# Kernel optimization log

Hardware: AMD Instinct MI355X
Metric: run time of the kernel (lower is better)

## Reference

```python
import jax, jax.numpy as jnp
import numpy as np
import math

D_MODEL = 1024
NUM_HEADS = 16
D_K = D_MODEL // NUM_HEADS
THETA = 10000.0
BATCH = 2
SEQ = 2048


def _trunc_normal(key, shape, std):
    # truncated normal in [-3std, 3std], matching torch.nn.init.trunc_normal_
    return jax.random.truncated_normal(key, -3.0, 3.0, shape, jnp.float32) * std


def setup_inputs() -> dict:
    key = jax.random.key(0)
    kx, kq, kk, kv, ko = jax.random.split(key, 5)
    std = math.sqrt(2.0 / (D_MODEL + D_MODEL))
    return {
        "x": jax.random.normal(kx, (BATCH, SEQ, D_MODEL), jnp.float32),
        "Wq": _trunc_normal(kq, (D_MODEL, D_MODEL), std),
        "Wk": _trunc_normal(kk, (D_MODEL, D_MODEL), std),
        "Wv": _trunc_normal(kv, (D_MODEL, D_MODEL), std),
        "Wo": _trunc_normal(ko, (D_MODEL, D_MODEL), std),
    }


def _apply_rope(t):
    # t: [B, H, S, d_k]; positions = arange(S)
    S = t.shape[-2]
    inv_freq = 1.0 / THETA ** (jnp.arange(0, D_K, 2, dtype=jnp.float32) / D_K)
    ang = jnp.arange(S, dtype=jnp.float32)[:, None] * inv_freq[None, :]  # [S, d_k/2]
    cos, sin = jnp.cos(ang), jnp.sin(ang)
    t1 = t[..., ::2]
    t2 = t[..., 1::2]
    r1 = t1 * cos - t2 * sin
    r2 = t1 * sin + t2 * cos
    # interleave back: even indices <- r1, odd <- r2
    out = jnp.stack([r1, r2], axis=-1).reshape(t.shape)
    return out


def reference(x, Wq, Wk, Wv, Wo):
    B, S, _ = x.shape
    def proj(W):
        return (x @ W.T).reshape(B, S, NUM_HEADS, D_K).transpose(0, 2, 1, 3)
    q = _apply_rope(proj(Wq))
    k = _apply_rope(proj(Wk))
    v = proj(Wv)
    scores = jnp.einsum('bhqd,bhkd->bhqk', q, k) / math.sqrt(D_K)
    causal = jnp.tril(jnp.ones((S, S), dtype=bool))
    scores = jnp.where(causal, scores, -jnp.inf)
    attn = jax.nn.softmax(scores, axis=-1)
    ctx = jnp.einsum('bhqk,bhkd->bhqd', attn, v)  # [B,H,S,d_k]
    ctx = ctx.transpose(0, 2, 1, 3).reshape(B, S, D_MODEL)
    return ctx @ Wo.T
```

## Files before the change

kernel.cpp:

```cpp
#include <hip/hip_runtime.h>
#include <hip/hip_bf16.h>


typedef __attribute__((ext_vector_type(8))) short bf16x8;
typedef __attribute__((ext_vector_type(4))) short bf16x4;
typedef __attribute__((ext_vector_type(4))) float f32x4;

#define D_MODEL 1024
#define SEQ     2048
#define NHEAD   16
#define DK      64
#define EXP_BIAS 16.0f

__device__ __forceinline__ f32x4 mfma16(bf16x8 a, bf16x8 b, f32x4 c) {
    return __builtin_amdgcn_mfma_f32_16x16x32_bf16(a, b, c, 0, 0, 0);
}

__device__ __forceinline__ void load_lds16(const __hip_bfloat16* g, __hip_bfloat16* l) {
    __builtin_amdgcn_global_load_lds((const __attribute__((address_space(1))) void*)g,
                                     (__attribute__((address_space(3))) void*)l,
                                     16, 0, 0);
}

__device__ __forceinline__ void cvt8(const float* p, __hip_bfloat16* dst) {
    const float4 f0 = *(const float4*)p;
    const float4 f1 = *(const float4*)(p + 4);
    alignas(16) __hip_bfloat16 t[8] = {
        __float2bfloat16(f0.x), __float2bfloat16(f0.y),
        __float2bfloat16(f0.z), __float2bfloat16(f0.w),
        __float2bfloat16(f1.x), __float2bfloat16(f1.y),
        __float2bfloat16(f1.z), __float2bfloat16(f1.w)};
    *(bf16x8*)dst = *(const bf16x8*)t;
}

__global__ __launch_bounds__(256) void cvt5_k(const float* __restrict__ wq,
                                              const float* __restrict__ wk,
                                              const float* __restrict__ wv,
                                              const float* __restrict__ wo,
                                              const float* __restrict__ x,
                                              __hip_bfloat16* __restrict__ dw,
                                              __hip_bfloat16* __restrict__ dwo,
                                              __hip_bfloat16* __restrict__ dx) {
    const int id = blockIdx.x;
    const float* s;
    __hip_bfloat16* d;
    int off;
    if (id < 1536)      { const int w = id >> 9; s = (w == 0) ? wq : (w == 1 ? wk : wv);
                          d = dw + (size_t)w * 1024 * 1024; off = (id & 511) * 2048; }
    else if (id < 2048) { s = wo; d = dwo; off = (id - 1536) * 2048; }
    else                { s = x;  d = dx;  off = (id - 2048) * 2048; }
    const int i = off + threadIdx.x * 8;
    alignas(16) __hip_bfloat16 t[8];
    cvt8(s + i, t);
    *(bf16x8*)(d + i) = *(const bf16x8*)t;
}

__global__ __launch_bounds__(256) void cvt3_k(const float* __restrict__ s0,
                                              const float* __restrict__ s1,
                                              const float* __restrict__ s2,
                                              __hip_bfloat16* __restrict__ d0,
                                              __hip_bfloat16* __restrict__ d1,
                                              __hip_bfloat16* __restrict__ d2) {
    const float* s = (blockIdx.y == 0) ? s0 : (blockIdx.y == 1 ? s1 : s2);
    __hip_bfloat16* d = (blockIdx.y == 0) ? d0 : (blockIdx.y == 1 ? d1 : d2);
    const int i = (blockIdx.x * 256 + threadIdx.x) * 8;
    alignas(16) __hip_bfloat16 t[8];
    cvt8(s + i, t);
    *(bf16x8*)(d + i) = *(const bf16x8*)t;
}

__device__ __forceinline__ void qkv_epilogue(f32x4 (&acc)[4][4], int wsel,
                                             int bm, int bn, int wave,
                                             int quad, int l15,
                                             __hip_bfloat16* Cq,
                                             __hip_bfloat16* Ck,
                                             __hip_bfloat16* Vt) {
    if (wsel < 2) {
        __hip_bfloat16* C = (wsel == 0) ? Cq : Ck;
#pragma unroll
        for (int i = 0; i < 4; ++i)
#pragma unroll
            for (int j = 0; j < 4; ++j)
#pragma unroll
                for (int r = 0; r < 4; ++r) {
                    const int row = bm + (wave >> 1) * 64 + i * 16 + quad * 4 + r;
                    const int col = bn + (wave & 1) * 64 + j * 16 + l15;
                    C[(size_t)row * 1024 + col] = __float2bfloat16(acc[i][j][r]);
                }
    } else {
#pragma unroll
        for (int i = 0; i < 4; ++i)
#pragma unroll
            for (int j = 0; j < 4; ++j) {
                const int col  = bn + (wave & 1) * 64 + j * 16 + l15;
                const int hh   = col >> 6, dd = col & 63;
                const int row0 = bm + (wave >> 1) * 64 + i * 16 + quad * 4;
                const int bb   = row0 >> 11, s0 = row0 & 2047;
                alignas(8) __hip_bfloat16 t4[4] = {
                    __float2bfloat16(acc[i][j][0]), __float2bfloat16(acc[i][j][1]),
                    __float2bfloat16(acc[i][j][2]), __float2bfloat16(acc[i][j][3])};
                *(uint2*)&Vt[((size_t)(bb * 16 + hh) * 64 + dd) * 2048 + s0] =
                    *(const uint2*)t4;
            }
    }
}

__global__ __launch_bounds__(256) void gemm_qkv_bf(const __hip_bfloat16* __restrict__ X,
                                                   const __hip_bfloat16* __restrict__ W,
                                                   __hip_bfloat16* __restrict__ Cq,
                                                   __hip_bfloat16* __restrict__ Ck,
                                                   __hip_bfloat16* __restrict__ Vt) {
    __shared__ alignas(16) __hip_bfloat16 a_lds[128 * 32];
    __shared__ alignas(16) __hip_bfloat16 b_lds[128 * 32];

    const int tid  = threadIdx.x;
    const int wave = tid >> 6;
    const int lane = tid & 63;
    const int quad = lane >> 4;
    const int l15  = lane & 15;

    const int wsel = blockIdx.x >> 3;
    const int bn   = (blockIdx.x & 7) * 128;
    const int bm   = blockIdx.y * 128;

    const __hip_bfloat16* B = W + (size_t)wsel * 1024 * 1024;

    f32x4 acc[4][4] = {};

    for (int k0 = 0; k0 < 1024; k0 += 32) {
        __syncthreads();
#pragma unroll
        for (int c = 0; c < 2; ++c) {
            const int chunk = (wave * 2 + c) * 64 + lane;
            const int row = chunk >> 2;
            const int col = (chunk & 3) * 8;
            load_lds16(&X[(size_t)(bm + row) * 1024 + k0 + col],
                       &a_lds[(wave * 2 + c) * 512]);
            load_lds16(&B[(size_t)(bn + row) * 1024 + k0 + col],
                       &b_lds[(wave * 2 + c) * 512]);
        }
        __syncthreads();

        bf16x8 af[4], bfr[4];
#pragma unroll
        for (int i = 0; i < 4; ++i)
            af[i] = *(const bf16x8*)&a_lds[((wave >> 1) * 64 + i * 16 + l15) * 32 + quad * 8];
#pragma unroll
        for (int j = 0; j < 4; ++j)
            bfr[j] = *(const bf16x8*)&b_lds[((wave & 1) * 64 + j * 16 + l15) * 32 + quad * 8];
#pragma unroll
        for (int i = 0; i < 4; ++i)
#pragma unroll
            for (int j = 0; j < 4; ++j)
                acc[i][j] = mfma16(af[i], bfr[j], acc[i][j]);
    }

    qkv_epilogue(acc, wsel, bm, bn, wave, quad, l15, Cq, Ck, Vt);
}

__global__ __launch_bounds__(256) void gemm_qkv_f32(const float* __restrict__ X,
                                                    const __hip_bfloat16* __restrict__ W,
                                                    __hip_bfloat16* __restrict__ Cq,
                                                    __hip_bfloat16* __restrict__ Ck,
                                                    __hip_bfloat16* __restrict__ Vt) {
    __shared__ alignas(16) __hip_bfloat16 a_lds[128 * 32];
    __shared__ alignas(16) __hip_bfloat16 b_lds[128 * 32];

    const int tid  = threadIdx.x;
    const int wave = tid >> 6;
    const int lane = tid & 63;
    const int quad = lane >> 4;
    const int l15  = lane & 15;

    const int wsel = blockIdx.x >> 3;
    const int bn   = (blockIdx.x & 7) * 128;
    const int bm   = blockIdx.y * 128;

    const __hip_bfloat16* B = W + (size_t)wsel * 1024 * 1024;

    f32x4 acc[4][4] = {};

    for (int k0 = 0; k0 < 1024; k0 += 32) {
        __syncthreads();
#pragma unroll
        for (int c = 0; c < 2; ++c) {
            const int e   = (c * 256 + tid) * 8;
            const int row = e >> 5;
            const int col = e & 31;
            cvt8(&X[(size_t)(bm + row) * 1024 + k0 + col], &a_lds[e]);
        }
#pragma unroll
        for (int c = 0; c < 2; ++c) {
            const int chunk = (wave * 2 + c) * 64 + lane;
            const int row = chunk >> 2;
            const int col = (chunk & 3) * 8;
            load_lds16(&B[(size_t)(bn + row) * 1024 + k0 + col],
                       &b_lds[(wave * 2 + c) * 512]);
        }
        __syncthreads();

        bf16x8 af[4], bfr[4];
#pragma unroll
        for (int i = 0; i < 4; ++i)
            af[i] = *(const bf16x8*)&a_lds[((wave >> 1) * 64 + i * 16 + l15) * 32 + quad * 8];
#pragma unroll
        for (int j = 0; j < 4; ++j)
            bfr[j] = *(const bf16x8*)&b_lds[((wave & 1) * 64 + j * 16 + l15) * 32 + quad * 8];
#pragma unroll
        for (int i = 0; i < 4; ++i)
#pragma unroll
            for (int j = 0; j < 4; ++j)
                acc[i][j] = mfma16(af[i], bfr[j], acc[i][j]);
    }

    qkv_epilogue(acc, wsel, bm, bn, wave, quad, l15, Cq, Ck, Vt);
}

__global__ __launch_bounds__(128) void gemm_o(const __hip_bfloat16* __restrict__ A,
                                              const __hip_bfloat16* __restrict__ B,
                                              float* __restrict__ C) {
    __shared__ alignas(16) __hip_bfloat16 a_lds[128 * 32];
    __shared__ alignas(16) __hip_bfloat16 b_lds[64 * 32];

    const int tid  = threadIdx.x;
    const int wave = tid >> 6;
    const int lane = tid & 63;
    const int quad = lane >> 4;
    const int l15  = lane & 15;

    const int bn = blockIdx.x * 64;
    const int bm = blockIdx.y * 128;

    f32x4 acc[4][4] = {};

    for (int k0 = 0; k0 < 1024; k0 += 32) {
        __syncthreads();
#pragma unroll
        for (int c = 0; c < 4; ++c) {
            const int chunk = (wave * 4 + c) * 64 + lane;
            const int row = chunk >> 2;
            const int col = (chunk & 3) * 8;
            load_lds16(&A[(size_t)(bm + row) * 1024 + k0 + col],
                       &a_lds[(wave * 4 + c) * 512]);
        }
#pragma unroll
        for (int c = 0; c < 2; ++c) {
            const int chunk = (wave * 2 + c) * 64 + lane;
            const int row = chunk >> 2;
            const int col = (chunk & 3) * 8;
            load_lds16(&B[(size_t)(bn + row) * 1024 + k0 + col],
                       &b_lds[(wave * 2 + c) * 512]);
        }
        __syncthreads();

        bf16x8 af[4], bfr[4];
#pragma unroll
        for (int i = 0; i < 4; ++i)
            af[i] = *(const bf16x8*)&a_lds[(wave * 64 + i * 16 + l15) * 32 + quad * 8];
#pragma unroll
        for (int j = 0; j < 4; ++j)
            bfr[j] = *(const bf16x8*)&b_lds[(j * 16 + l15) * 32 + quad * 8];
#pragma unroll
        for (int i = 0; i < 4; ++i)
#pragma unroll
            for (int j = 0; j < 4; ++j)
                acc[i][j] = mfma16(af[i], bfr[j], acc[i][j]);
    }

#pragma unroll
    for (int i = 0; i < 4; ++i)
#pragma unroll
        for (int j = 0; j < 4; ++j)
#pragma unroll
            for (int r = 0; r < 4; ++r) {
                const int row = bm + wave * 64 + i * 16 + quad * 4 + r;
                const int col = bn + j * 16 + l15;
                C[(size_t)row * 1024 + col] = acc[i][j][r];
            }
}

__global__ __launch_bounds__(256) void rope_k(__hip_bfloat16* Q, __hip_bfloat16* K) {
    const int idx = blockIdx.x * 256 + threadIdx.x;
    const int row = idx >> 7;
    const int g   = idx & 127;
    const int col = g * 8;
    const int s   = row & (SEQ - 1);
    const int i0  = (g & 7) * 4;

    float sn[4], cs[4];
#pragma unroll
    for (int z = 0; z < 4; ++z) {
        const float ang = (float)s * __expf(-(float)(i0 + z) * 0.28782313663f);
        __sincosf(ang, &sn[z], &cs[z]);
    }

    const size_t o = (size_t)row * D_MODEL + col;
    alignas(16) __hip_bfloat16 q8[8], k8[8];
    *(uint4*)q8 = *(const uint4*)&Q[o];
    *(uint4*)k8 = *(const uint4*)&K[o];
#pragma unroll
    for (int z = 0; z < 4; ++z) {
        const float q1 = __bfloat162float(q8[2 * z]);
        const float q2 = __bfloat162float(q8[2 * z + 1]);
        q8[2 * z]     = __float2bfloat16((q1 * cs[z] - q2 * sn[z]) * 0.125f);
        q8[2 * z + 1] = __float2bfloat16((q1 * sn[z] + q2 * cs[z]) * 0.125f);
        const float k1 = __bfloat162float(k8[2 * z]);
        const float k2 = __bfloat162float(k8[2 * z + 1]);
        k8[2 * z]     = __float2bfloat16(k1 * cs[z] - k2 * sn[z]);
        k8[2 * z + 1] = __float2bfloat16(k1 * sn[z] + k2 * cs[z]);
    }
    *(uint4*)&Q[o] = *(const uint4*)q8;
    *(uint4*)&K[o] = *(const uint4*)k8;
}

__global__ __launch_bounds__(256, 4) void attn_k(const __hip_bfloat16* Q,
                                                 const __hip_bfloat16* K,
                                                 const __hip_bfloat16* Vt,
                                                 __hip_bfloat16* O) {
    __shared__ alignas(16) __hip_bfloat16 k_s[2][64 * 72];
    __shared__ alignas(16) __hip_bfloat16 vt_s[2][64 * 72];

    const int tid  = threadIdx.x;
    const int wave = tid >> 6;
    const int lane = tid & 63;
    const int quad = lane >> 4;
    const int l15  = lane & 15;

    const int hw = blockIdx.x;
    const int j  = hw >> 3;
    const int g  = j >> 5;
    const int m  = j & 31;
    const int bh = (hw & 7) * 4 + g;
    const int qt = (g & 1) ? m : (31 - m);
    const int b  = bh >> 4;
    const int h  = bh & 15;
    const int q0 = qt * 64;

    const int r0 = tid >> 3;
    const int d8 = (tid & 7) * 8;

    const size_t vtBase = (size_t)bh * (64 * 2048);

    {
        const size_t baseK = ((size_t)(b * SEQ)) * D_MODEL + h * DK;
#pragma unroll
        for (int c = 0; c < 2; ++c) {
            const int row = r0 + c * 32;
            const uint4 kv = *(const uint4*)&K[baseK + (size_t)row * D_MODEL + d8];
            const uint4 vv = *(const uint4*)&Vt[vtBase + (size_t)row * 2048 + d8];
            *(uint4*)&k_s[0][row * 72 + d8] = kv;
            *(uint4*)&vt_s[0][row * 72 + d8] = vv;
        }
    }

    bf16x8 qa0, qa1;
    {
        const size_t baseQ = ((size_t)(b * SEQ + q0 + wave * 16 + l15)) * D_MODEL + h * DK;
        qa0 = *(const bf16x8*)&Q[baseQ + quad * 8];
        qa1 = *(const bf16x8*)&Q[baseQ + 32 + quad * 8];
    }
    __syncthreads();

    float l4[4] = {0.f, 0.f, 0.f, 0.f};
    f32x4 o_acc[4] = {};

    for (int kt = 0; kt <= qt; ++kt) {
        const int buf = kt & 1;
        const bool pf = (kt < qt);
        uint4 kr0, kr1, vr0, vr1;
        if (pf) {
            const size_t baseK = ((size_t)(b * SEQ + (kt + 1) * 64)) * D_MODEL + h * DK;
            const size_t baseV = vtBase + (size_t)(kt + 1) * 64;
            kr0 = *(const uint4*)&K[baseK + (size_t)r0 * D_MODEL + d8];
            kr1 = *(const uint4*)&K[baseK + (size_t)(r0 + 32) * D_MODEL + d8];
            vr0 = *(const uint4*)&Vt[baseV + (size_t)r0 * 2048 + d8];
            vr1 = *(const uint4*)&Vt[baseV + (size_t)(r0 + 32) * 2048 + d8];
        }

        const bool diag = (kt == qt);
        alignas(16) __hip_bfloat16 pk0[8], pk1[8];
#pragma unroll
        for (int t = 0; t < 4; ++t) {
            __hip_bfloat16* dst = (t < 2) ? pk0 : pk1;
            const int zo = (t & 1) * 4;
            if (diag && t > wave) {
#pragma unroll
                for (int r = 0; r < 4; ++r) dst[zo + r] = __float2bfloat16(0.0f);
                continue;
            }
            f32x4 a = {};
            {
                const bf16x8 kb0 = *(const bf16x8*)&k_s[buf][(t * 16 + l15) * 72 + quad * 8];
                a = mfma16(kb0, qa0, a);
                const bf16x8 kb1 = *(const bf16x8*)&k_s[buf][(t * 16 + l15) * 72 + 32 + quad * 8];
                a = mfma16(kb1, qa1, a);
            }
#pragma unroll
            for (int r = 0; r < 4; ++r) {
                float v = a[r];
                if (diag && t == wave && (quad * 4 + r > l15)) v = -1e30f;
                const float pv = __expf(v - EXP_BIAS);
                l4[r] += pv;
                dst[zo + r] = __float2bfloat16(pv);
            }
        }
        const bf16x8 pa0 = *(const bf16x8*)pk0;
        const bf16x8 pa1 = *(const bf16x8*)pk1;

        if (pf) {
            *(uint4*)&k_s[buf ^ 1][r0 * 72 + d8] = kr0;
            *(uint4*)&k_s[buf ^ 1][(r0 + 32) * 72 + d8] = kr1;
            *(uint4*)&vt_s[buf ^ 1][r0 * 72 + d8] = vr0;
            *(uint4*)&vt_s[buf ^ 1][(r0 + 32) * 72 + d8] = vr1;
        }

#pragma unroll
        for (int ks = 0; ks < 2; ++ks) {
            if (diag && ks == 1 && wave < 2) continue;
            const bf16x8 pa = ks ? pa1 : pa0;
#pragma unroll
            for (int t2 = 0; t2 < 4; ++t2) {
                const int vb = (t2 * 16 + l15) * 72 + ks * 32 + quad * 4;
                const bf16x4 lo = *(const bf16x4*)&vt_s[buf][vb];
                const bf16x4 hi = *(const bf16x4*)&vt_s[buf][vb + 16];
                bf16x8 vv;
#pragma unroll
                for (int z = 0; z < 4; ++z) { vv[z] = lo[z]; vv[z + 4] = hi[z]; }
                o_acc[t2] = mfma16(pa, vv, o_acc[t2]);
            }
        }

        __syncthreads();
    }

    float l_loc = (l4[0] + l4[1]) + (l4[2] + l4[3]);
    l_loc += __shfl_xor(l_loc, 16);
    l_loc += __shfl_xor(l_loc, 32);
    float lr[4];
#pragma unroll
    for (int r = 0; r < 4; ++r) lr[r] = __shfl(l_loc, quad * 4 + r);

#pragma unroll
    for (int t2 = 0; t2 < 4; ++t2)
#pragma unroll
        for (int r = 0; r < 4; ++r) {
            const int row = q0 + wave * 16 + quad * 4 + r;
            const int d   = t2 * 16 + l15;
            O[((size_t)(b * SEQ + row)) * D_MODEL + h * DK + d] =
                __float2bfloat16(o_acc[t2][r] / lr[r]);
        }
}

extern "C" void kernel_launch(void* const* d_in, const int* in_sizes, int n_in,
                              void* d_out, int out_size, void* d_ws, size_t ws_size,
                              hipStream_t stream) {
    const float* x  = (const float*)d_in[0];
    const float* Wq = (const float*)d_in[1];
    const float* Wk = (const float*)d_in[2];
    const float* Wv = (const float*)d_in[3];
    const float* Wo = (const float*)d_in[4];

    const size_t MT = (size_t)4096 * 1024;
    const size_t WT = (size_t)1024 * 1024;
    __hip_bfloat16* Qw = (__hip_bfloat16*)d_ws;
    __hip_bfloat16* Vt = Qw + MT;
    __hip_bfloat16* Wb = (__hip_bfloat16*)d_out;
    __hip_bfloat16* Kw = (__hip_bfloat16*)((char*)d_out + 8 * 1024 * 1024);

    const bool big = ws_size >= (size_t)26 * 1024 * 1024;

    if (big) {
        __hip_bfloat16* xb  = Qw + 2 * MT;
        __hip_bfloat16* WoB = (__hip_bfloat16*)((char*)d_ws + 24 * 1024 * 1024);
        cvt5_k<<<4096, 256, 0, stream>>>(Wq, Wk, Wv, Wo, x, Wb, WoB, xb);
        gemm_qkv_bf<<<dim3(24, 32), 256, 0, stream>>>(xb, Wb, Qw, Kw, Vt);
        rope_k<<<(4096 * 128) / 256, 256, 0, stream>>>(Qw, Kw);
        attn_k<<<dim3(1024), 256, 0, stream>>>(Qw, Kw, Vt, Qw);
        gemm_o<<<dim3(16, 32), 128, 0, stream>>>(Qw, WoB, (float*)d_out);
    } else {
        __hip_bfloat16* WoB = Vt;
        cvt3_k<<<dim3(512, 3), 256, 0, stream>>>(Wq, Wk, Wv, Wb, Wb + WT, Wb + 2 * WT);
        gemm_qkv_f32<<<dim3(24, 32), 256, 0, stream>>>(x, Wb, Qw, Kw, Vt);
        rope_k<<<(4096 * 128) / 256, 256, 0, stream>>>(Qw, Kw);
        attn_k<<<dim3(1024), 256, 0, stream>>>(Qw, Kw, Vt, Qw);
        cvt3_k<<<dim3(512, 1), 256, 0, stream>>>(Wo, Wo, Wo, WoB, WoB, WoB);
        gemm_o<<<dim3(16, 32), 128, 0, stream>>>(Qw, WoB, (float*)d_out);
    }
}
```

Before: 186.6 us.

## Permute V^T in LDS for single 16-byte reads and peel diagonal tile

Stores the V^T tile into LDS in a permuted column order so each lane can read its 8-element MFMA operand with one 16-byte load instead of two 8-byte loads plus a shuffle. The diagonal key tile is peeled out of the main loop, so the steady-state loop runs without masking and prefetch branches. The query-tile assignment for the upper half of the heads is rotated to spread causal work more evenly across blocks. The trade-off is extra address arithmetic and split 8-byte LDS stores when filling V^T.

```diff
diff --git a/kernel.cpp b/kernel.cpp
--- a/kernel.cpp
+++ b/kernel.cpp
@@ -331,26 +331,31 @@
     const int g  = j >> 5;
     const int m  = j & 31;
     const int bh = (hw & 7) * 4 + g;
-    const int qt = (g & 1) ? m : (31 - m);
+    const int mm = (g >= 2) ? ((m + 8) & 31) : m;
+    const int qt = (g & 1) ? mm : (31 - mm);
     const int b  = bh >> 4;
     const int h  = bh & 15;
     const int q0 = qt * 64;
 
     const int r0 = tid >> 3;
     const int d8 = (tid & 7) * 8;
+    const int vp0 = ((d8 >> 5) << 5) + (((d8 & 15) >> 2) << 3) + (((d8 >> 4) & 1) << 2);
+    const int d4  = d8 + 4;
+    const int vp1 = ((d4 >> 5) << 5) + (((d4 & 15) >> 2) << 3) + (((d4 >> 4) & 1) << 2);
 
     const size_t vtBase = (size_t)bh * (64 * 2048);
-
-    {
-        const size_t baseK = ((size_t)(b * SEQ)) * D_MODEL + h * DK;
-#pragma unroll
-        for (int c = 0; c < 2; ++c) {
-            const int row = r0 + c * 32;
-            const uint4 kv = *(const uint4*)&K[baseK + (size_t)row * D_MODEL + d8];
-            const uint4 vv = *(const uint4*)&Vt[vtBase + (size_t)row * 2048 + d8];
-            *(uint4*)&k_s[0][row * 72 + d8] = kv;
-            *(uint4*)&vt_s[0][row * 72 + d8] = vv;
-        }
+    const size_t baseK0 = ((size_t)(b * SEQ)) * D_MODEL + h * DK;
+
+#pragma unroll
+    for (int c = 0; c < 2; ++c) {
+        const int row = r0 + c * 32;
+        const uint4 kv = *(const uint4*)&K[baseK0 + (size_t)row * D_MODEL + d8];
+        const uint4 vv = *(const uint4*)&Vt[vtBase + (size_t)row * 2048 + d8];
+        *(uint4*)&k_s[0][row * 72 + d8] = kv;
+        uint2 lo, hi;
+        lo.x = vv.x; lo.y = vv.y; hi.x = vv.z; hi.y = vv.w;
+        *(uint2*)&vt_s[0][row * 72 + vp0] = lo;
+        *(uint2*)&vt_s[0][row * 72 + vp1] = hi;
     }
 
     bf16x8 qa0, qa1;
@@ -364,12 +369,12 @@
     float l4[4] = {0.f, 0.f, 0.f, 0.f};
     f32x4 o_acc[4] = {};
 
-    for (int kt = 0; kt <= qt; ++kt) {
+    for (int kt = 0; kt < qt; ++kt) {
         const int buf = kt & 1;
-        const bool pf = (kt < qt);
+
         uint4 kr0, kr1, vr0, vr1;
-        if (pf) {
-            const size_t baseK = ((size_t)(b * SEQ + (kt + 1) * 64)) * D_MODEL + h * DK;
+        {
+            const size_t baseK = baseK0 + (size_t)(kt + 1) * 64 * D_MODEL;
             const size_t baseV = vtBase + (size_t)(kt + 1) * 64;
             kr0 = *(const uint4*)&K[baseK + (size_t)r0 * D_MODEL + d8];
             kr1 = *(const uint4*)&K[baseK + (size_t)(r0 + 32) * D_MODEL + d8];
@@ -377,28 +382,73 @@
             vr1 = *(const uint4*)&Vt[baseV + (size_t)(r0 + 32) * 2048 + d8];
         }
 
-        const bool diag = (kt == qt);
         alignas(16) __hip_bfloat16 pk0[8], pk1[8];
 #pragma unroll
         for (int t = 0; t < 4; ++t) {
             __hip_bfloat16* dst = (t < 2) ? pk0 : pk1;
             const int zo = (t & 1) * 4;
-            if (diag && t > wave) {
+            f32x4 a = {};
+            const bf16x8 kb0 = *(const bf16x8*)&k_s[buf][(t * 16 + l15) * 72 + quad * 8];
+            a = mfma16(kb0, qa0, a);
+            const bf16x8 kb1 = *(const bf16x8*)&k_s[buf][(t * 16 + l15) * 72 + 32 + quad * 8];
+            a = mfma16(kb1, qa1, a);
+#pragma unroll
+            for (int r = 0; r < 4; ++r) {
+                const float pv = __expf(a[r] - EXP_BIAS);
+                l4[r] += pv;
+                dst[zo + r] = __float2bfloat16(pv);
+            }
+        }
+        const bf16x8 pa0 = *(const bf16x8*)pk0;
+        const bf16x8 pa1 = *(const bf16x8*)pk1;
+
+#pragma unroll
+        for (int ks = 0; ks < 2; ++ks) {
+            const bf16x8 pa = ks ? pa1 : pa0;
+#pragma unroll
+            for (int t2 = 0; t2 < 4; ++t2) {
+                const bf16x8 vv = *(const bf16x8*)
+                    &vt_s[buf][(t2 * 16 + l15) * 72 + ks * 32 + quad * 8];
+                o_acc[t2] = mfma16(pa, vv, o_acc[t2]);
+            }
+        }
+
+        *(uint4*)&k_s[buf ^ 1][r0 * 72 + d8] = kr0;
+        *(uint4*)&k_s[buf ^ 1][(r0 + 32) * 72 + d8] = kr1;
+        {
+            uint2 lo0, hi0, lo1, hi1;
+            lo0.x = vr0.x; lo0.y = vr0.y; hi0.x = vr0.z; hi0.y = vr0.w;
+            lo1.x = vr1.x; lo1.y = vr1.y; hi1.x = vr1.z; hi1.y = vr1.w;
+            *(uint2*)&vt_s[buf ^ 1][r0 * 72 + vp0] = lo0;
+            *(uint2*)&vt_s[buf ^ 1][r0 * 72 + vp1] = hi0;
+            *(uint2*)&vt_s[buf ^ 1][(r0 + 32) * 72 + vp0] = lo1;
+            *(uint2*)&vt_s[buf ^ 1][(r0 + 32) * 72 + vp1] = hi1;
+        }
+
+        __syncthreads();
+    }
+
+    {
+        const int buf = qt & 1;
+        alignas(16) __hip_bfloat16 pk0[8], pk1[8];
+#pragma unroll
+        for (int t = 0; t < 4; ++t) {
+            __hip_bfloat16* dst = (t < 2) ? pk0 : pk1;
+            const int zo = (t & 1) * 4;
+            if (t > wave) {
 #pragma unroll
                 for (int r = 0; r < 4; ++r) dst[zo + r] = __float2bfloat16(0.0f);
                 continue;
             }
             f32x4 a = {};
-            {
-                const bf16x8 kb0 = *(const bf16x8*)&k_s[buf][(t * 16 + l15) * 72 + quad * 8];
-                a = mfma16(kb0, qa0, a);
-                const bf16x8 kb1 = *(const bf16x8*)&k_s[buf][(t * 16 + l15) * 72 + 32 + quad * 8];
-                a = mfma16(kb1, qa1, a);
-            }
+            const bf16x8 kb0 = *(const bf16x8*)&k_s[buf][(t * 16 + l15) * 72 + quad * 8];
+            a = mfma16(kb0, qa0, a);
+            const bf16x8 kb1 = *(const bf16x8*)&k_s[buf][(t * 16 + l15) * 72 + 32 + quad * 8];
+            a = mfma16(kb1, qa1, a);
 #pragma unroll
             for (int r = 0; r < 4; ++r) {
                 float v = a[r];
-                if (diag && t == wave && (quad * 4 + r > l15)) v = -1e30f;
+                if (t == wave && (quad * 4 + r > l15)) v = -1e30f;
                 const float pv = __expf(v - EXP_BIAS);
                 l4[r] += pv;
                 dst[zo + r] = __float2bfloat16(pv);
@@ -407,30 +457,17 @@
         const bf16x8 pa0 = *(const bf16x8*)pk0;
         const bf16x8 pa1 = *(const bf16x8*)pk1;
 
-        if (pf) {
-            *(uint4*)&k_s[buf ^ 1][r0 * 72 + d8] = kr0;
-            *(uint4*)&k_s[buf ^ 1][(r0 + 32) * 72 + d8] = kr1;
-            *(uint4*)&vt_s[buf ^ 1][r0 * 72 + d8] = vr0;
-            *(uint4*)&vt_s[buf ^ 1][(r0 + 32) * 72 + d8] = vr1;
-        }
-
 #pragma unroll
         for (int ks = 0; ks < 2; ++ks) {
-            if (diag && ks == 1 && wave < 2) continue;
+            if (ks == 1 && wave < 2) continue;
             const bf16x8 pa = ks ? pa1 : pa0;
 #pragma unroll
             for (int t2 = 0; t2 < 4; ++t2) {
-                const int vb = (t2 * 16 + l15) * 72 + ks * 32 + quad * 4;
-                const bf16x4 lo = *(const bf16x4*)&vt_s[buf][vb];
-                const bf16x4 hi = *(const bf16x4*)&vt_s[buf][vb + 16];
-                bf16x8 vv;
-#pragma unroll
-                for (int z = 0; z < 4; ++z) { vv[z] = lo[z]; vv[z + 4] = hi[z]; }
+                const bf16x8 vv = *(const bf16x8*)
+                    &vt_s[buf][(t2 * 16 + l15) * 72 + ks * 32 + quad * 8];
                 o_acc[t2] = mfma16(pa, vv, o_acc[t2]);
             }
         }
-
-        __syncthreads();
     }
 
     float l_loc = (l4[0] + l4[1]) + (l4[2] + l4[3]);
```

New measurement: 181.9 us (median of 2 runs). -2.5%, faster.
